# Kernel tuning notes

Measured on AMD Instinct MI355X. Metric: run time of the kernel, lower is better.

The kernel has to match this reference:

```python
import jax, jax.numpy as jnp
import numpy as np

ALPHA = 0.2  # LeakyReLU negative slope

def setup_inputs() -> dict:
    key = jax.random.key(0)
    k1, k2, k3 = jax.random.split(key, 3)
    B, N, D_in, D_out = 4, 512, 512, 256
    H = jax.random.normal(k1, (B, N, D_in), dtype=jnp.float32)
    # xavier-style scaled params
    W = jax.random.normal(k2, (D_out, D_in), dtype=jnp.float32) * (2.0 / (D_in + D_out)) ** 0.5
    a = jax.random.normal(k3, (D_out, 1), dtype=jnp.float32) * (2.0 / (D_out + 1)) ** 0.5
    return {"H": H, "W": W, "a": a}

def reference(H, W, a):
    # Wh: [B, N, D_out]
    Wh = jnp.einsum('bnd,od->bno', H, W)
    # additive pairwise scores: e[b,i,j] = leakyrelu(Wh[b,i]+Wh[b,j]) . a
    e = jnp.einsum('bijo,o->bij',
                   jax.nn.leaky_relu(Wh[:, :, None, :] + Wh[:, None, :, :], ALPHA),
                   a[:, 0])
    attention = jax.nn.softmax(e, axis=-1)          # [B, N, N]
    H_att = jnp.einsum('bij,bjo->bio', attention, Wh)  # [B, N, D_out]
    return H_att
```

## Files before the change

### kernel.cpp

```cpp
#include <hip/hip_runtime.h>

constexpr int Bq   = 4;
constexpr int Nq   = 512;
constexpr int DIN  = 512;
constexpr int DOUT = 256;

typedef _Float16 h2  __attribute__((ext_vector_type(2)));
typedef _Float16 h4  __attribute__((ext_vector_type(4)));
typedef _Float16 h8  __attribute__((ext_vector_type(8)));
typedef float    f4v __attribute__((ext_vector_type(4)));

#if defined(__has_builtin) && __has_builtin(__builtin_amdgcn_fdot2)
__device__ __forceinline__ float fdot2f(h2 a, h2 b, float c) {
    return __builtin_amdgcn_fdot2(a, b, c, false);
}
#else
__device__ __forceinline__ float fdot2f(h2 a, h2 b, float c) {
    return (float)a.x * (float)b.x + (float)a.y * (float)b.y + c;
}
#endif

__device__ __forceinline__ h8 cvt8(float4 lo, float4 hi) {
    h8 r;
    r[0] = (_Float16)lo.x; r[1] = (_Float16)lo.y;
    r[2] = (_Float16)lo.z; r[3] = (_Float16)lo.w;
    r[4] = (_Float16)hi.x; r[5] = (_Float16)hi.y;
    r[6] = (_Float16)hi.z; r[7] = (_Float16)hi.w;
    return r;
}

__global__ __launch_bounds__(256) void k1_wh(const float* __restrict__ H,
                                             const float* __restrict__ W,
                                             const float* __restrict__ a,
                                             h2* __restrict__ Wh16,
                                             h2* __restrict__ WhT16p,
                                             h2* __restrict__ WhT16n,
                                             h2* __restrict__ a16) {
    const int bid = blockIdx.x;
    const int t   = threadIdx.x;

    if (bid == 1024) {
        if (t < 64) {
            const int idx = 2 * t;
            const float4 v = *(const float4*)&a[2 * idx];
            h2 h0; h0.x = (_Float16)v.x; h0.y = (_Float16)v.y;
            h2 h1; h1.x = (_Float16)v.z; h1.y = (_Float16)v.w;
            a16[idx] = h0; a16[idx + 1] = h1;
        }
        return;
    }

    const int w    = t >> 6;
    const int lane = t & 63;
    const int T    = (bid << 1) | (w & 1);
    const int kh   = w >> 1;
    const int mt   = T >> 4;
    const int b    = mt & 3;
    const int n0   = (T >> 6) << 4;
    const int o0   = (T & 15) << 4;
    const int quad = lane >> 4;
    const int col  = lane & 15;

    const float4* __restrict__ aP =
        (const float4*)(H + (size_t)(b * Nq + n0 + col) * DIN) + kh * 64 + quad * 2;
    const float4* __restrict__ bP =
        (const float4*)(W + (size_t)(o0 + col) * DIN) + kh * 64 + quad * 2;

    f4v acc = {0.f, 0.f, 0.f, 0.f};
    float4 fa0 = aP[0], fa1 = aP[1];
    float4 fb0 = bP[0], fb1 = bP[1];

#pragma unroll
    for (int kb = 0; kb < 8; ++kb) {
        float4 na0 = fa0, na1 = fa1, nb0 = fb0, nb1 = fb1;
        if (kb < 7) {
            na0 = aP[(kb + 1) * 8];
            na1 = aP[(kb + 1) * 8 + 1];
            nb0 = bP[(kb + 1) * 8];
            nb1 = bP[(kb + 1) * 8 + 1];
        }
        const h8 af = cvt8(fa0, fa1);
        const h8 bf = cvt8(fb0, fb1);
        acc = __builtin_amdgcn_mfma_f32_16x16x32_f16(af, bf, acc, 0, 0, 0);
        fa0 = na0; fa1 = na1; fb0 = nb0; fb1 = nb1;
    }

    __shared__ f4v sPart[2][64];
    if (kh) sPart[w & 1][lane] = acc;
    __syncthreads();
    if (!kh) {
        const f4v p = sPart[w & 1][lane];
#pragma unroll
        for (int r = 0; r < 4; ++r) acc[r] += p[r];

        const int rloc = n0 + quad * 4;

        h4 hj;
        hj[0] = (_Float16)acc[0]; hj[1] = (_Float16)acc[1];
        hj[2] = (_Float16)acc[2]; hj[3] = (_Float16)acc[3];
        *(h4*)(WhT16n + ((size_t)(b * 256 + o0 + col)) * 256 + (rloc >> 1)) = hj;

#pragma unroll
        for (int reg = 0; reg < 4; ++reg) {
            const float v  = acc[reg];
            const float vp = __shfl_xor(v, 1);
            if ((col & 1) == 0) {
                h2 hv; hv.x = (_Float16)v; hv.y = (_Float16)vp;
                const int o2 = (o0 + col) >> 1;
                Wh16[(size_t)(b * Nq + rloc + reg) * 128 + o2] = hv;
                WhT16p[(size_t)b * 65536 + (size_t)o2 * 512 + (rloc + reg)] = hv;
            }
        }
    }
}

__global__ __launch_bounds__(1024, 8) void k23(const h2* __restrict__ Wh16,
                                               const h2* __restrict__ WhT16p,
                                               const h2* __restrict__ WhT16n,
                                               const h2* __restrict__ a16,
                                               float* __restrict__ out) {
    const int t   = threadIdx.x;
    const int blk = blockIdx.x;
    const int b   = blk & 3;
    const int i0  = (blk >> 2) << 3;

    __shared__ float smem[5120];
    __shared__ h2    sPh[8 * 260];
    __shared__ float wred[2][8][8];

    {
        const int h  = __builtin_amdgcn_readfirstlane(t >> 9);
        const int j  = t & 511;
        const int ob = h * 64;

        const h2* __restrict__ wjp = WhT16p + (size_t)b * 65536 + (size_t)ob * 512 + j;
        const h2* __restrict__ wip = Wh16 + (size_t)(b * Nq + i0) * 128;

        float ab[8];
#pragma unroll
        for (int rr = 0; rr < 8; ++rr) ab[rr] = 0.f;
        float rja = 0.f;
        h2 cA[8], cB[8];

#define K2_L8(buf, kb)                                                      \
    _Pragma("unroll") for (int s = 0; s < 8; ++s)                           \
        buf[s] = wjp[((kb) + s) * 512];

#define K2_C8(buf, kb)                                                      \
    _Pragma("unroll") for (int s = 0; s < 8; ++s) {                         \
        const int o2 = ob + (kb) + s;                                       \
        const h2 a2 = a16[o2];                                  \
        rja = fdot2f(a2, buf[s], rja);                                      \
        _Pragma("unroll") for (int rr = 0; rr < 8; ++rr) {                  \
            const h2 wi = wip[rr * 128 + o2];                   \
            h2 w  = buf[s] + wi;                                \
            h2 aw = __builtin_elementwise_max(w, -w);           \
            ab[rr] = fdot2f(a2, aw, ab[rr]);                    \
        }                                                                   \
    }

        K2_L8(cA, 0)  K2_L8(cB, 8)
        K2_C8(cA, 0)  K2_L8(cA, 16)
        K2_C8(cB, 8)  K2_L8(cB, 24)
        K2_C8(cA, 16) K2_L8(cA, 32)
        K2_C8(cB, 24) K2_L8(cB, 40)
        K2_C8(cA, 32) K2_L8(cA, 48)
        K2_C8(cB, 40) K2_L8(cB, 56)
        K2_C8(cA, 48)
        K2_C8(cB, 56)
#undef K2_L8
#undef K2_C8

        float* sAb = smem;
        float* sRh = smem + 4096;
        float* sRf = smem + 4608;
        if (h == 1) {
#pragma unroll
            for (int rr = 0; rr < 8; ++rr) sAb[rr * 512 + j] = ab[rr];
            sRh[j] = rja;
        }
        __syncthreads();

        float rj = 0.f;
        if (h == 0) {
#pragma unroll
            for (int rr = 0; rr < 8; ++rr) ab[rr] += sAb[rr * 512 + j];
            rj = rja + sRh[j];
            sRf[j] = rj;
        }
        __syncthreads();

        float e[8], pv[8];
        const int lane = t & 63;
        const int w    = t >> 6;

        if (h == 0) {
#pragma unroll
            for (int rr = 0; rr < 8; ++rr)
                e[rr] = 0.6f * (sRf[i0 + rr] + rj) + 0.4f * ab[rr];
#pragma unroll
            for (int rr = 0; rr < 8; ++rr) {
                float v = e[rr];
#pragma unroll
                for (int off = 32; off > 0; off >>= 1) v = fmaxf(v, __shfl_xor(v, off));
                if (lane == 0) wred[0][rr][w] = v;
            }
        }
        __syncthreads();
        if (h == 0) {
#pragma unroll
            for (int rr = 0; rr < 8; ++rr) {
                const float4 q0 = *(const float4*)&wred[0][rr][0];
                const float4 q1 = *(const float4*)&wred[0][rr][4];
                const float m = fmaxf(fmaxf(fmaxf(q0.x, q0.y), fmaxf(q0.z, q0.w)),
                                      fmaxf(fmaxf(q1.x, q1.y), fmaxf(q1.z, q1.w)));
                pv[rr] = __expf(e[rr] - m);
            }
#pragma unroll
            for (int rr = 0; rr < 8; ++rr) {
                float v = pv[rr];
#pragma unroll
                for (int off = 32; off > 0; off >>= 1) v += __shfl_xor(v, off);
                if (lane == 0) wred[1][rr][w] = v;
            }
        }
        __syncthreads();
        if (h == 0) {
#pragma unroll
            for (int rr = 0; rr < 8; ++rr) {
                const float4 q0 = *(const float4*)&wred[1][rr][0];
                const float4 q1 = *(const float4*)&wred[1][rr][4];
                const float s = (q0.x + q0.y + q0.z + q0.w) + (q1.x + q1.y + q1.z + q1.w);
                const float pn = pv[rr] * (1.0f / s);
                const float pp = __shfl_xor(pn, 1);
                if ((j & 1) == 0) {
                    h2 hv; hv.x = (_Float16)pn; hv.y = (_Float16)pp;
                    sPh[rr * 260 + (j >> 1)] = hv;
                }
            }
        }
        __syncthreads();
    }

    {
        const int w16  = __builtin_amdgcn_readfirstlane(t >> 6);
        const int lane = t & 63;
        const int quad = lane >> 4;
        const int col  = lane & 15;
        const int o0   = w16 << 4;

        const h2* __restrict__ wt =
            WhT16n + (size_t)b * 65536 + (size_t)(o0 + col) * 256 + quad * 4;
        const h2* __restrict__ ap = sPh + (col & 7) * 260 + quad * 4;

        f4v acc = {0.f, 0.f, 0.f, 0.f};
        h8 b0 = *(const h8*)wt;
#pragma unroll
        for (int kb = 0; kb < 16; ++kb) {
            h8 b1 = b0;
            if (kb < 15) b1 = *(const h8*)(wt + (kb + 1) * 16);
            const h8 af = *(const h8*)(ap + kb * 16);
            acc = __builtin_amdgcn_mfma_f32_16x16x32_f16(af, b0, acc, 0, 0, 0);
            b0 = b1;
        }

        if (quad < 2) {
#pragma unroll
            for (int reg = 0; reg < 4; ++reg) {
                const int row = quad * 4 + reg;
                out[((size_t)(b * Nq) + i0 + row) * DOUT + o0 + col] = acc[reg];
            }
        }
    }
}

extern "C" void kernel_launch(void* const* d_in, const int* in_sizes, int n_in,
                              void* d_out, int out_size, void* d_ws, size_t ws_size,
                              hipStream_t stream) {
    const float* H = (const float*)d_in[0];
    const float* W = (const float*)d_in[1];
    const float* a = (const float*)d_in[2];
    float* out = (float*)d_out;

    h2* Wh16   = (h2*)d_ws;
    h2* WhT16p = Wh16 + 262144;
    h2* WhT16n = WhT16p + 262144;
    h2* a16    = WhT16n + 262144;

    hipLaunchKernelGGL(k1_wh, dim3(1025), dim3(256),  0, stream, H, W, a, Wh16, WhT16p, WhT16n, a16);
    hipLaunchKernelGGL(k23,   dim3(256),  dim3(1024), 0, stream, Wh16, WhT16p, WhT16n, a16, out);
}
```

Before: 107.5 us.

## Drop split-K in Wh GEMM and halve rows per attention block

The Wh projection kernel drops its two-way K split and shared-memory reduction: each of its 4 waves now computes a full-K 16x16 tile, and the grid is halved. The attention kernel processes 4 query rows per block instead of 8, doubling the grid to 512 blocks so more CUs are busy. The trade is that every Wh^T column and the a vector are reloaded twice as often, and half of the MFMA rows in the final product are wasted.

```diff
diff --git a/kernel.cpp b/kernel.cpp
--- a/kernel.cpp
+++ b/kernel.cpp
@@ -39,7 +39,7 @@
     const int bid = blockIdx.x;
     const int t   = threadIdx.x;
 
-    if (bid == 1024) {
+    if (bid == 512) {
         if (t < 64) {
             const int idx = 2 * t;
             const float4 v = *(const float4*)&a[2 * idx];
@@ -52,28 +52,26 @@
 
     const int w    = t >> 6;
     const int lane = t & 63;
-    const int T    = (bid << 1) | (w & 1);
-    const int kh   = w >> 1;
-    const int mt   = T >> 4;
+    const int mt   = bid >> 2;
     const int b    = mt & 3;
-    const int n0   = (T >> 6) << 4;
-    const int o0   = (T & 15) << 4;
+    const int n0   = (mt >> 2) << 4;
+    const int o0   = ((bid & 3) << 6) + (w << 4);
     const int quad = lane >> 4;
     const int col  = lane & 15;
 
     const float4* __restrict__ aP =
-        (const float4*)(H + (size_t)(b * Nq + n0 + col) * DIN) + kh * 64 + quad * 2;
+        (const float4*)(H + (size_t)(b * Nq + n0 + col) * DIN) + quad * 2;
     const float4* __restrict__ bP =
-        (const float4*)(W + (size_t)(o0 + col) * DIN) + kh * 64 + quad * 2;
+        (const float4*)(W + (size_t)(o0 + col) * DIN) + quad * 2;
 
     f4v acc = {0.f, 0.f, 0.f, 0.f};
     float4 fa0 = aP[0], fa1 = aP[1];
     float4 fb0 = bP[0], fb1 = bP[1];
 
 #pragma unroll
-    for (int kb = 0; kb < 8; ++kb) {
+    for (int kb = 0; kb < 16; ++kb) {
         float4 na0 = fa0, na1 = fa1, nb0 = fb0, nb1 = fb1;
-        if (kb < 7) {
+        if (kb < 15) {
             na0 = aP[(kb + 1) * 8];
             na1 = aP[(kb + 1) * 8 + 1];
             nb0 = bP[(kb + 1) * 8];
@@ -85,31 +83,22 @@
         fa0 = na0; fa1 = na1; fb0 = nb0; fb1 = nb1;
     }
 
-    __shared__ f4v sPart[2][64];
-    if (kh) sPart[w & 1][lane] = acc;
-    __syncthreads();
-    if (!kh) {
-        const f4v p = sPart[w & 1][lane];
-#pragma unroll
-        for (int r = 0; r < 4; ++r) acc[r] += p[r];
-
-        const int rloc = n0 + quad * 4;
-
-        h4 hj;
-        hj[0] = (_Float16)acc[0]; hj[1] = (_Float16)acc[1];
-        hj[2] = (_Float16)acc[2]; hj[3] = (_Float16)acc[3];
-        *(h4*)(WhT16n + ((size_t)(b * 256 + o0 + col)) * 256 + (rloc >> 1)) = hj;
-
-#pragma unroll
-        for (int reg = 0; reg < 4; ++reg) {
-            const float v  = acc[reg];
-            const float vp = __shfl_xor(v, 1);
-            if ((col & 1) == 0) {
-                h2 hv; hv.x = (_Float16)v; hv.y = (_Float16)vp;
-                const int o2 = (o0 + col) >> 1;
-                Wh16[(size_t)(b * Nq + rloc + reg) * 128 + o2] = hv;
-                WhT16p[(size_t)b * 65536 + (size_t)o2 * 512 + (rloc + reg)] = hv;
-            }
+    const int rloc = n0 + quad * 4;
+
+    h4 hj;
+    hj[0] = (_Float16)acc[0]; hj[1] = (_Float16)acc[1];
+    hj[2] = (_Float16)acc[2]; hj[3] = (_Float16)acc[3];
+    *(h4*)(WhT16n + ((size_t)(b * 256 + o0 + col)) * 256 + (rloc >> 1)) = hj;
+
+#pragma unroll
+    for (int reg = 0; reg < 4; ++reg) {
+        const float v  = acc[reg];
+        const float vp = __shfl_xor(v, 1);
+        if ((col & 1) == 0) {
+            h2 hv; hv.x = (_Float16)v; hv.y = (_Float16)vp;
+            const int o2 = (o0 + col) >> 1;
+            Wh16[(size_t)(b * Nq + rloc + reg) * 128 + o2] = hv;
+            WhT16p[(size_t)b * 65536 + (size_t)o2 * 512 + (rloc + reg)] = hv;
         }
     }
 }
@@ -122,11 +111,11 @@
     const int t   = threadIdx.x;
     const int blk = blockIdx.x;
     const int b   = blk & 3;
-    const int i0  = (blk >> 2) << 3;
-
-    __shared__ float smem[5120];
-    __shared__ h2    sPh[8 * 260];
-    __shared__ float wred[2][8][8];
+    const int i0  = (blk >> 2) << 2;
+
+    __shared__ float smem[8192];
+    __shared__ __align__(16) h2 sPh[4 * 272];
+    __shared__ float wred[2][4][8];
 
     {
         const int h  = __builtin_amdgcn_readfirstlane(t >> 9);
@@ -136,9 +125,7 @@
         const h2* __restrict__ wjp = WhT16p + (size_t)b * 65536 + (size_t)ob * 512 + j;
         const h2* __restrict__ wip = Wh16 + (size_t)(b * Nq + i0) * 128;
 
-        float ab[8];
-#pragma unroll
-        for (int rr = 0; rr < 8; ++rr) ab[rr] = 0.f;
+        float ab[4] = {0.f, 0.f, 0.f, 0.f};
         float rja = 0.f;
         h2 cA[8], cB[8];
 
@@ -151,7 +138,7 @@
         const int o2 = ob + (kb) + s;                                       \
         const h2 a2 = a16[o2];                                  \
         rja = fdot2f(a2, buf[s], rja);                                      \
-        _Pragma("unroll") for (int rr = 0; rr < 8; ++rr) {                  \
+        _Pragma("unroll") for (int rr = 0; rr < 4; ++rr) {                  \
             const h2 wi = wip[rr * 128 + o2];                   \
             h2 w  = buf[s] + wi;                                \
             h2 aw = __builtin_elementwise_max(w, -w);           \
@@ -172,11 +159,11 @@
 #undef K2_C8
 
         float* sAb = smem;
-        float* sRh = smem + 4096;
-        float* sRf = smem + 4608;
+        float* sRh = smem + 2048;
+        float* sRf = smem + 2560;
         if (h == 1) {
 #pragma unroll
-            for (int rr = 0; rr < 8; ++rr) sAb[rr * 512 + j] = ab[rr];
+            for (int rr = 0; rr < 4; ++rr) sAb[rr * 512 + j] = ab[rr];
             sRh[j] = rja;
         }
         __syncthreads();
@@ -184,22 +171,22 @@
         float rj = 0.f;
         if (h == 0) {
 #pragma unroll
-            for (int rr = 0; rr < 8; ++rr) ab[rr] += sAb[rr * 512 + j];
+            for (int rr = 0; rr < 4; ++rr) ab[rr] += sAb[rr * 512 + j];
             rj = rja + sRh[j];
             sRf[j] = rj;
         }
         __syncthreads();
 
-        float e[8], pv[8];
+        float e[4], pv[4];
         const int lane = t & 63;
         const int w    = t >> 6;
 
         if (h == 0) {
 #pragma unroll
-            for (int rr = 0; rr < 8; ++rr)
+            for (int rr = 0; rr < 4; ++rr)
                 e[rr] = 0.6f * (sRf[i0 + rr] + rj) + 0.4f * ab[rr];
 #pragma unroll
-            for (int rr = 0; rr < 8; ++rr) {
+            for (int rr = 0; rr < 4; ++rr) {
                 float v = e[rr];
 #pragma unroll
                 for (int off = 32; off > 0; off >>= 1) v = fmaxf(v, __shfl_xor(v, off));
@@ -209,7 +196,7 @@
         __syncthreads();
         if (h == 0) {
 #pragma unroll
-            for (int rr = 0; rr < 8; ++rr) {
+            for (int rr = 0; rr < 4; ++rr) {
                 const float4 q0 = *(const float4*)&wred[0][rr][0];
                 const float4 q1 = *(const float4*)&wred[0][rr][4];
                 const float m = fmaxf(fmaxf(fmaxf(q0.x, q0.y), fmaxf(q0.z, q0.w)),
@@ -217,7 +204,7 @@
                 pv[rr] = __expf(e[rr] - m);
             }
 #pragma unroll
-            for (int rr = 0; rr < 8; ++rr) {
+            for (int rr = 0; rr < 4; ++rr) {
                 float v = pv[rr];
 #pragma unroll
                 for (int off = 32; off > 0; off >>= 1) v += __shfl_xor(v, off);
@@ -227,7 +214,7 @@
         __syncthreads();
         if (h == 0) {
 #pragma unroll
-            for (int rr = 0; rr < 8; ++rr) {
+            for (int rr = 0; rr < 4; ++rr) {
                 const float4 q0 = *(const float4*)&wred[1][rr][0];
                 const float4 q1 = *(const float4*)&wred[1][rr][4];
                 const float s = (q0.x + q0.y + q0.z + q0.w) + (q1.x + q1.y + q1.z + q1.w);
@@ -235,7 +222,7 @@
                 const float pp = __shfl_xor(pn, 1);
                 if ((j & 1) == 0) {
                     h2 hv; hv.x = (_Float16)pn; hv.y = (_Float16)pp;
-                    sPh[rr * 260 + (j >> 1)] = hv;
+                    sPh[rr * 272 + (j >> 1)] = hv;
                 }
             }
         }
@@ -251,7 +238,7 @@
 
         const h2* __restrict__ wt =
             WhT16n + (size_t)b * 65536 + (size_t)(o0 + col) * 256 + quad * 4;
-        const h2* __restrict__ ap = sPh + (col & 7) * 260 + quad * 4;
+        const h2* __restrict__ ap = sPh + (col & 3) * 272 + quad * 4;
 
         f4v acc = {0.f, 0.f, 0.f, 0.f};
         h8 b0 = *(const h8*)wt;
@@ -264,11 +251,10 @@
             b0 = b1;
         }
 
-        if (quad < 2) {
+        if (quad == 0) {
 #pragma unroll
             for (int reg = 0; reg < 4; ++reg) {
-                const int row = quad * 4 + reg;
-                out[((size_t)(b * Nq) + i0 + row) * DOUT + o0 + col] = acc[reg];
+                out[((size_t)(b * Nq) + i0 + reg) * DOUT + o0 + col] = acc[reg];
             }
         }
     }
@@ -287,6 +273,6 @@
     h2* WhT16n = WhT16p + 262144;
     h2* a16    = WhT16n + 262144;
 
-    hipLaunchKernelGGL(k1_wh, dim3(1025), dim3(256),  0, stream, H, W, a, Wh16, WhT16p, WhT16n, a16);
-    hipLaunchKernelGGL(k23,   dim3(256),  dim3(1024), 0, stream, Wh16, WhT16p, WhT16n, a16, out);
-}
+    hipLaunchKernelGGL(k1_wh, dim3(513), dim3(256),  0, stream, H, W, a, Wh16, WhT16p, WhT16n, a16);
+    hipLaunchKernelGGL(k23,   dim3(512), dim3(1024), 0, stream, Wh16, WhT16p, WhT16n, a16, out);
+}
```

New measurement: 107.0 us. Within noise of the previous version (-0.5%).
